# Optimization experiments

Measured on AMD Instinct MI355X. Metric: run time of the kernel, lower is better.

The kernel has to match this reference:

```python
import jax, jax.numpy as jnp
import numpy as np

N = 20000
E = 320000
CIN = 16
COUT = 16
D = 4
RADIUS = 0.5


def setup_inputs() -> dict:
    key = jax.random.key(0)
    k1, k2, k3, k4 = jax.random.split(key, 4)
    positions = jax.random.uniform(k1, (N, 3), dtype=jnp.float32)
    features = jax.random.normal(k2, (N, CIN), dtype=jnp.float32)
    filters = jax.random.normal(k3, (D, D, D, CIN, COUT), dtype=jnp.float32)
    edge_index = jax.random.randint(k4, (2, E), 0, N, dtype=jnp.int32)
    return {"positions": positions, "features": features,
            "filters": filters, "edge_index": edge_index}


def _trilinear(filters, gc):
    # Replicates torch grid_sample(align_corners=True) semantics used by the
    # module: grid coord (x,y,z) indexes spatial dims (W,H,D), i.e. gc[:,0]
    # samples filter axis 2, gc[:,1] axis 1, gc[:,2] axis 0.
    Dres = filters.shape[0]
    a, b, c = gc[:, 2], gc[:, 1], gc[:, 0]  # axes 0, 1, 2 of filters
    a0f, b0f, c0f = jnp.floor(a), jnp.floor(b), jnp.floor(c)
    a0 = jnp.clip(a0f.astype(jnp.int32), 0, Dres - 1)
    b0 = jnp.clip(b0f.astype(jnp.int32), 0, Dres - 1)
    c0 = jnp.clip(c0f.astype(jnp.int32), 0, Dres - 1)
    a1 = jnp.minimum(a0 + 1, Dres - 1)
    b1 = jnp.minimum(b0 + 1, Dres - 1)
    c1 = jnp.minimum(c0 + 1, Dres - 1)
    ad = (a - a0f)[:, None, None]  # (E,1,1)
    bd = (b - b0f)[:, None, None]
    cd = (c - c0f)[:, None, None]

    g = lambda i, j, k: filters[i, j, k]  # (E, CIN, COUT) gather
    f00 = g(a0, b0, c0) * (1 - cd) + g(a0, b0, c1) * cd
    f01 = g(a0, b1, c0) * (1 - cd) + g(a0, b1, c1) * cd
    f10 = g(a1, b0, c0) * (1 - cd) + g(a1, b0, c1) * cd
    f11 = g(a1, b1, c0) * (1 - cd) + g(a1, b1, c1) * cd
    f0 = f00 * (1 - bd) + f01 * bd
    f1 = f10 * (1 - bd) + f11 * bd
    return f0 * (1 - ad) + f1 * ad  # (E, CIN, COUT)


def reference(positions, features, filters, edge_index):
    row, col = edge_index[0], edge_index[1]
    r = positions[col] - positions[row]                  # (E,3)
    dist2 = jnp.sum(r * r, axis=-1)                      # (E,)
    valid = (dist2 < RADIUS ** 2).astype(positions.dtype)
    window = (1.0 - dist2 / RADIUS ** 2) ** 3 * valid
    norm = jnp.sqrt(dist2)[:, None]
    mapped = r / (norm + 1e-8) * jnp.tanh(norm)          # ball -> cube, (E,3)
    gc = (mapped + 1.0) * ((filters.shape[0] - 1) / 2.0) # (E,3) in [0, D-1]
    filt = _trilinear(filters, gc)                       # (E, CIN, COUT)
    conv_edge = jnp.einsum('eio,ei->eo', filt, features[col])
    conv_edge = conv_edge * window[:, None]
    n_nodes = positions.shape[0]
    sums = jax.ops.segment_sum(conv_edge, row, num_segments=n_nodes)
    cnt = jax.ops.segment_sum(jnp.ones((conv_edge.shape[0],), positions.dtype),
                              row, num_segments=n_nodes)
    return sums / jnp.maximum(cnt, 1.0)[:, None]         # scatter-mean
```

## Files before the change

kernel.cpp:

```cpp
#include <hip/hip_runtime.h>
#include <hip/hip_fp16.h>
#include <math.h>

#define NN 20000
#define EE 320000
#define CIN 16
#define COUT 16
#define R2C 0.25f

#define WS_NEED 81920

typedef _Float16 h2 __attribute__((ext_vector_type(2)));

#if defined(__has_builtin)
# if __has_builtin(__builtin_amdgcn_fdot2)
#  define HAS_FDOT2 1
# endif
#endif
#ifndef HAS_FDOT2
# define HAS_FDOT2 0
#endif

__device__ __forceinline__ h2 as_h2(unsigned int x) {
    union { unsigned int u; h2 h; } v; v.u = x; return v.h;
}
__device__ __forceinline__ h2 pk(float a, float b) {
    h2 r; r.x = (_Float16)a; r.y = (_Float16)b; return r;
}
__device__ __forceinline__ unsigned int pku(float a, float b) {
    __half2 h = __float22half2_rn(make_float2(a, b));
    return *(unsigned int*)&h;
}

__global__ __launch_bounds__(256) void k_zero(float* __restrict__ out, int* __restrict__ cnt) {
    int i = blockIdx.x * 256 + threadIdx.x;
    if (i < NN * COUT) out[i] = 0.0f;
    if (i < NN) cnt[i] = 0;
}

__global__ __launch_bounds__(256) void k_edge(const float* __restrict__ pos,
                                              const int* __restrict__ ei,
                                              const float* __restrict__ feat,
                                              const float* __restrict__ filt,
                                              float* __restrict__ out,
                                              int* __restrict__ cnts) {
    __shared__ uint4 sf[2048];
    {
        #pragma unroll
        for (int r = 0; r < 8; ++r) {
            int g = r * 256 + threadIdx.x;
            const float* src = filt + (g >> 4) * 128 + (g & 15);
            float s0 = src[0],  s1 = src[16],  s2 = src[32],  s3 = src[48];
            float s4 = src[64], s5 = src[80],  s6 = src[96],  s7 = src[112];
            uint4 v;
            v.x = pku(s0, s1); v.y = pku(s2, s3);
            v.z = pku(s4, s5); v.w = pku(s6, s7);
            sf[g] = v;
        }
    }
    __syncthreads();

    int lane = threadIdx.x & 63;
    int gid  = lane >> 4;
    int o    = lane & 15;
    int wv   = threadIdx.x >> 6;

    #pragma unroll
    for (int ch = 0; ch < 2; ++ch) {
        int e = blockIdx.x * 512 + ch * 256 + wv * 64 + lane;

        int row = ei[e];
        int col = ei[EE + e];
        atomicAdd(&cnts[row], 1);

        float rx = pos[col*3+0] - pos[row*3+0];
        float ry = pos[col*3+1] - pos[row*3+1];
        float rz = pos[col*3+2] - pos[row*3+2];
        float d2 = rx*rx + ry*ry + rz*rz;
        bool valid = d2 < R2C;

        float win = 0.f, ad = 0.f, bd = 0.f, cd = 0.f;
        int colidx = 0;
        if (valid) {
            float u = 1.0f - d2 * 4.0f;
            win = u * u * u;
            float s = 1.0f + d2*(-0.33333333f + d2*(0.13333333f + d2*(-0.05396825f + d2*0.02186949f)));
            float gx = (rx * s + 1.0f) * 1.5f;
            float gy = (ry * s + 1.0f) * 1.5f;
            float gz = (rz * s + 1.0f) * 1.5f;
            float af = floorf(gz), bf = floorf(gy), cf = floorf(gx);
            int ia0 = min(max((int)af, 0), 2);
            int jb0 = min(max((int)bf, 0), 2);
            int kc0 = min(max((int)cf, 0), 2);
            ad = gz - af; bd = gy - bf; cd = gx - cf;
            colidx = col | (ia0 << 20) | (jb0 << 24) | (kc0 << 28);
        }

        unsigned long long bal = __ballot(valid);
        int nv = __popcll(bal);
        unsigned long long m0 = bal;
        unsigned long long m1 = m0 & (m0 - 1);
        unsigned long long m2 = m1 & (m1 - 1);
        unsigned long long m3 = m2 & (m2 - 1);

        for (int k = 0; k < nv; k += 4) {
            unsigned long long mg = (gid == 0) ? m0 : (gid == 1) ? m1 : (gid == 2) ? m2 : m3;
            bool active = (k + gid) < nv;
            int src = active ? (int)__builtin_ctzll(mg) : 0;

            float win_s = __shfl(win, src, 64);
            float ad_s  = __shfl(ad,  src, 64);
            float bd_s  = __shfl(bd,  src, 64);
            float cd_s  = __shfl(cd,  src, 64);
            int   ci_s  = __shfl(colidx, src, 64);
            int   row_s = __shfl(row,    src, 64);

            m0 = m3 & (m3 - 1);
            m1 = m0 & (m0 - 1);
            m2 = m1 & (m1 - 1);
            m3 = m2 & (m2 - 1);

            if (active) {
                int col_s = ci_s & 0xFFFFF;
                int ia0 = (ci_s >> 20) & 3, jb0 = (ci_s >> 24) & 3, kc0 = (ci_s >> 28) & 3;

                const float4* fb = (const float4*)(feat + (size_t)col_s * 16);
                float4 fa = fb[0], fc = fb[1], fd = fb[2], fe = fb[3];

                float va0 = (1.f - ad_s) * win_s, va1 = ad_s * win_s;
                float vb0 = 1.f - bd_s, vb1 = bd_s;
                float vc0 = 1.f - cd_s, vc1 = cd_s;
                float p00 = va0*vb0, p01 = va0*vb1, p10 = va1*vb0, p11 = va1*vb1;
                float w8[8] = { p00*vc0, p00*vc1, p01*vc0, p01*vc1,
                                p10*vc0, p10*vc1, p11*vc0, p11*vc1 };

                int bi = ((ia0 * 16 + jb0 * 4 + kc0) << 5) + o;
                const int cofs[8] = {0, 32, 128, 160, 512, 544, 640, 672};

                float acc = 0.f;
#if HAS_FDOT2
                h2 ft0 = pk(fa.x, fa.y), ft1 = pk(fa.z, fa.w);
                h2 ft2 = pk(fc.x, fc.y), ft3 = pk(fc.z, fc.w);
                h2 ft4 = pk(fd.x, fd.y), ft5 = pk(fd.z, fd.w);
                h2 ft6 = pk(fe.x, fe.y), ft7 = pk(fe.z, fe.w);
                #pragma unroll
                for (int c = 0; c < 8; ++c) {
                    uint4 g0 = sf[bi + cofs[c]];
                    uint4 g1 = sf[bi + cofs[c] + 16];
                    float d = 0.f;
                    d = __builtin_amdgcn_fdot2(as_h2(g0.x), ft0, d, false);
                    d = __builtin_amdgcn_fdot2(as_h2(g0.y), ft1, d, false);
                    d = __builtin_amdgcn_fdot2(as_h2(g0.z), ft2, d, false);
                    d = __builtin_amdgcn_fdot2(as_h2(g0.w), ft3, d, false);
                    d = __builtin_amdgcn_fdot2(as_h2(g1.x), ft4, d, false);
                    d = __builtin_amdgcn_fdot2(as_h2(g1.y), ft5, d, false);
                    d = __builtin_amdgcn_fdot2(as_h2(g1.z), ft6, d, false);
                    d = __builtin_amdgcn_fdot2(as_h2(g1.w), ft7, d, false);
                    acc = fmaf(w8[c], d, acc);
                }
#else
                float ftf[16] = { fa.x, fa.y, fa.z, fa.w, fc.x, fc.y, fc.z, fc.w,
                                  fd.x, fd.y, fd.z, fd.w, fe.x, fe.y, fe.z, fe.w };
                #pragma unroll
                for (int c = 0; c < 8; ++c) {
                    uint4 g0 = sf[bi + cofs[c]];
                    uint4 g1 = sf[bi + cofs[c] + 16];
                    float d = 0.f;
                    h2 t;
                    t = as_h2(g0.x); d = fmaf((float)t.x, ftf[0],  d); d = fmaf((float)t.y, ftf[1],  d);
                    t = as_h2(g0.y); d = fmaf((float)t.x, ftf[2],  d); d = fmaf((float)t.y, ftf[3],  d);
                    t = as_h2(g0.z); d = fmaf((float)t.x, ftf[4],  d); d = fmaf((float)t.y, ftf[5],  d);
                    t = as_h2(g0.w); d = fmaf((float)t.x, ftf[6],  d); d = fmaf((float)t.y, ftf[7],  d);
                    t = as_h2(g1.x); d = fmaf((float)t.x, ftf[8],  d); d = fmaf((float)t.y, ftf[9],  d);
                    t = as_h2(g1.y); d = fmaf((float)t.x, ftf[10], d); d = fmaf((float)t.y, ftf[11], d);
                    t = as_h2(g1.z); d = fmaf((float)t.x, ftf[12], d); d = fmaf((float)t.y, ftf[13], d);
                    t = as_h2(g1.w); d = fmaf((float)t.x, ftf[14], d); d = fmaf((float)t.y, ftf[15], d);
                    acc = fmaf(w8[c], d, acc);
                }
#endif
                atomicAdd(out + (size_t)row_s * 16 + o, acc);
            }
        }
    }
}

__global__ __launch_bounds__(256) void k_div(float* __restrict__ out, const int* __restrict__ cnt) {
    int i = blockIdx.x * 256 + threadIdx.x;
    if (i >= NN * COUT) return;
    int c = cnt[i >> 4];
    float denom = (c > 1) ? (float)c : 1.0f;
    out[i] = out[i] / denom;
}

__device__ __forceinline__ bool edge_geom(const float* __restrict__ pos, int row, int col,
                                          float& win,
                                          int ia[2], int jb[2], int kc[2],
                                          float wa[2], float wb[2], float wc[2]) {
    float rx = pos[col*3+0] - pos[row*3+0];
    float ry = pos[col*3+1] - pos[row*3+1];
    float rz = pos[col*3+2] - pos[row*3+2];
    float d2 = rx*rx + ry*ry + rz*rz;
    if (!(d2 < R2C)) return false;
    float u = 1.0f - d2 / R2C;
    win = u * u * u;
    float nr = sqrtf(d2);
    float s  = tanhf(nr) / (nr + 1e-8f);
    float gx = (rx * s + 1.0f) * 1.5f;
    float gy = (ry * s + 1.0f) * 1.5f;
    float gz = (rz * s + 1.0f) * 1.5f;
    float af = floorf(gz), bf = floorf(gy), cf = floorf(gx);
    int ia0 = min(max((int)af, 0), 3);
    int ib0 = min(max((int)bf, 0), 3);
    int ic0 = min(max((int)cf, 0), 3);
    ia[0] = ia0; ia[1] = min(ia0 + 1, 3);
    jb[0] = ib0; jb[1] = min(ib0 + 1, 3);
    kc[0] = ic0; kc[1] = min(ic0 + 1, 3);
    float ad = gz - af, bd = gy - bf, cd = gx - cf;
    wa[0] = 1.0f - ad; wa[1] = ad;
    wb[0] = 1.0f - bd; wb[1] = bd;
    wc[0] = 1.0f - cd; wc[1] = cd;
    return true;
}

__global__ __launch_bounds__(256) void k_edge_direct(const float* __restrict__ pos,
                                                     const float* __restrict__ feat,
                                                     const float* __restrict__ filt,
                                                     const int* __restrict__ ei,
                                                     float* __restrict__ out,
                                                     int* __restrict__ cnt) {
    int e = blockIdx.x * 256 + threadIdx.x;
    if (e >= EE) return;
    int row = ei[e];
    int col = ei[EE + e];
    atomicAdd(&cnt[row], 1);

    float win;
    int ia[2], jb[2], kc[2];
    float wa[2], wb[2], wc[2];
    if (!edge_geom(pos, row, col, win, ia, jb, kc, wa, wb, wc)) return;

    float fv[16];
    const float4* fp = (const float4*)(feat + (size_t)col * 16);
    float4 f0 = fp[0], f1 = fp[1], f2 = fp[2], f3 = fp[3];
    fv[0]=f0.x; fv[1]=f0.y; fv[2]=f0.z; fv[3]=f0.w;
    fv[4]=f1.x; fv[5]=f1.y; fv[6]=f1.z; fv[7]=f1.w;
    fv[8]=f2.x; fv[9]=f2.y; fv[10]=f2.z; fv[11]=f2.w;
    fv[12]=f3.x; fv[13]=f3.y; fv[14]=f3.z; fv[15]=f3.w;

    float4 a0 = make_float4(0.f,0.f,0.f,0.f);
    float4 a1 = a0, a2 = a0, a3 = a0;
    for (int da = 0; da < 2; ++da)
    for (int db = 0; db < 2; ++db)
    for (int dc = 0; dc < 2; ++dc) {
        float w = wa[da] * wb[db] * wc[dc] * win;
        const float* fb = filt + (size_t)(ia[da]*16 + jb[db]*4 + kc[dc]) * 256;
        #pragma unroll
        for (int ci = 0; ci < 16; ++ci) {
            float c = w * fv[ci];
            const float4* r4 = (const float4*)(fb + ci * 16);
            float4 w0 = r4[0], w1 = r4[1], w2 = r4[2], w3 = r4[3];
            a0.x = fmaf(c, w0.x, a0.x); a0.y = fmaf(c, w0.y, a0.y);
            a0.z = fmaf(c, w0.z, a0.z); a0.w = fmaf(c, w0.w, a0.w);
            a1.x = fmaf(c, w1.x, a1.x); a1.y = fmaf(c, w1.y, a1.y);
            a1.z = fmaf(c, w1.z, a1.z); a1.w = fmaf(c, w1.w, a1.w);
            a2.x = fmaf(c, w2.x, a2.x); a2.y = fmaf(c, w2.y, a2.y);
            a2.z = fmaf(c, w2.z, a2.z); a2.w = fmaf(c, w2.w, a2.w);
            a3.x = fmaf(c, w3.x, a3.x); a3.y = fmaf(c, w3.y, a3.y);
            a3.z = fmaf(c, w3.z, a3.z); a3.w = fmaf(c, w3.w, a3.w);
        }
    }
    float* op = out + (size_t)row * 16;
    atomicAdd(op+0,  a0.x); atomicAdd(op+1,  a0.y); atomicAdd(op+2,  a0.z); atomicAdd(op+3,  a0.w);
    atomicAdd(op+4,  a1.x); atomicAdd(op+5,  a1.y); atomicAdd(op+6,  a1.z); atomicAdd(op+7,  a1.w);
    atomicAdd(op+8,  a2.x); atomicAdd(op+9,  a2.y); atomicAdd(op+10, a2.z); atomicAdd(op+11, a2.w);
    atomicAdd(op+12, a3.x); atomicAdd(op+13, a3.y); atomicAdd(op+14, a3.z); atomicAdd(op+15, a3.w);
}

extern "C" void kernel_launch(void* const* d_in, const int* in_sizes, int n_in,
                              void* d_out, int out_size, void* d_ws, size_t ws_size,
                              hipStream_t stream) {
    const float* pos  = (const float*)d_in[0];
    const float* feat = (const float*)d_in[1];
    const float* filt = (const float*)d_in[2];
    const int*   ei   = (const int*)d_in[3];
    float* out = (float*)d_out;

    int* cnts = (int*)d_ws;

    k_zero<<<(NN * COUT + 255) / 256, 256, 0, stream>>>(out, cnts);
    if (ws_size >= WS_NEED) {
        k_edge<<<625, 256, 0, stream>>>(pos, ei, feat, filt, out, cnts);
    } else {
        k_edge_direct<<<(EE + 255) / 256, 256, 0, stream>>>(pos, feat, filt, ei, out, cnts);
    }
    k_div<<<(NN * COUT + 255) / 256, 256, 0, stream>>>(out, cnts);
}
```

Baseline: 92.02 us.

## Prefetch edge indices before filter staging and software-pipeline lane shuffles

Edge index loads and count atomics for both 256-edge chunks are now issued before and alongside the shared-memory filter staging, so their global latency overlaps the LDS fill. Geometry for both chunks is computed up front, which lets the position gathers of the second chunk overlap with the first. Inside the compaction loop, the shuffles for the next round are issued before the current round's work, which hides cross-lane latency. The cost is higher register pressure from holding two edge states and the double-buffered shuffled values.

```diff
diff --git a/kernel.cpp b/kernel.cpp
--- a/kernel.cpp
+++ b/kernel.cpp
@@ -38,6 +38,142 @@
     if (i < NN) cnt[i] = 0;
 }
 
+struct EdgeSt {
+    float win, ad, bd, cd;
+    int colidx, row;
+    unsigned long long bal;
+};
+
+__device__ __forceinline__ void geom(const float* __restrict__ pos, int row, int col,
+                                     EdgeSt& st) {
+    float rx = pos[col*3+0] - pos[row*3+0];
+    float ry = pos[col*3+1] - pos[row*3+1];
+    float rz = pos[col*3+2] - pos[row*3+2];
+    float d2 = rx*rx + ry*ry + rz*rz;
+    bool valid = d2 < R2C;
+    st.win = 0.f; st.ad = 0.f; st.bd = 0.f; st.cd = 0.f; st.colidx = 0; st.row = row;
+    if (valid) {
+        float u = 1.0f - d2 * 4.0f;
+        st.win = u * u * u;
+        float s = 1.0f + d2*(-0.33333333f + d2*(0.13333333f + d2*(-0.05396825f + d2*0.02186949f)));
+        float gx = (rx * s + 1.0f) * 1.5f;
+        float gy = (ry * s + 1.0f) * 1.5f;
+        float gz = (rz * s + 1.0f) * 1.5f;
+        float af = floorf(gz), bf = floorf(gy), cf = floorf(gx);
+        int ia0 = min(max((int)af, 0), 2);
+        int jb0 = min(max((int)bf, 0), 2);
+        int kc0 = min(max((int)cf, 0), 2);
+        st.ad = gz - af; st.bd = gy - bf; st.cd = gx - cf;
+        st.colidx = col | (ia0 << 20) | (jb0 << 24) | (kc0 << 28);
+    }
+    st.bal = __ballot(valid);
+}
+
+__device__ __forceinline__ void conv_rounds(const EdgeSt& st,
+                                            const uint4* __restrict__ sf,
+                                            const float* __restrict__ feat,
+                                            float* __restrict__ out,
+                                            int gid, int o) {
+    unsigned long long bal = st.bal;
+    int nv = __popcll(bal);
+    if (nv == 0) return;
+
+    unsigned long long m0 = bal;
+    unsigned long long m1 = m0 & (m0 - 1);
+    unsigned long long m2 = m1 & (m1 - 1);
+    unsigned long long m3 = m2 & (m2 - 1);
+
+    unsigned long long mg = (gid == 0) ? m0 : (gid == 1) ? m1 : (gid == 2) ? m2 : m3;
+    int src = mg ? (int)__builtin_ctzll(mg) : 0;
+    float win_s = __shfl(st.win, src, 64);
+    float ad_s  = __shfl(st.ad,  src, 64);
+    float bd_s  = __shfl(st.bd,  src, 64);
+    float cd_s  = __shfl(st.cd,  src, 64);
+    int   ci_s  = __shfl(st.colidx, src, 64);
+    int   row_s = __shfl(st.row,    src, 64);
+
+    for (int k = 0; k < nv; k += 4) {
+        m0 = m3 & (m3 - 1);
+        m1 = m0 & (m0 - 1);
+        m2 = m1 & (m1 - 1);
+        m3 = m2 & (m2 - 1);
+        unsigned long long mg2 = (gid == 0) ? m0 : (gid == 1) ? m1 : (gid == 2) ? m2 : m3;
+        int src2 = mg2 ? (int)__builtin_ctzll(mg2) : 0;
+
+        bool active = (k + gid) < nv;
+        float winc = win_s, adc = ad_s, bdc = bd_s, cdc = cd_s;
+        int   cic = ci_s, rowc = row_s;
+
+        win_s = __shfl(st.win, src2, 64);
+        ad_s  = __shfl(st.ad,  src2, 64);
+        bd_s  = __shfl(st.bd,  src2, 64);
+        cd_s  = __shfl(st.cd,  src2, 64);
+        ci_s  = __shfl(st.colidx, src2, 64);
+        row_s = __shfl(st.row,    src2, 64);
+
+        if (active) {
+            int col_s = cic & 0xFFFFF;
+            int ia0 = (cic >> 20) & 3, jb0 = (cic >> 24) & 3, kc0 = (cic >> 28) & 3;
+
+            const float4* fb = (const float4*)(feat + (size_t)col_s * 16);
+            float4 fa = fb[0], fc = fb[1], fd = fb[2], fe = fb[3];
+
+            float va0 = (1.f - adc) * winc, va1 = adc * winc;
+            float vb0 = 1.f - bdc, vb1 = bdc;
+            float vc0 = 1.f - cdc, vc1 = cdc;
+            float p00 = va0*vb0, p01 = va0*vb1, p10 = va1*vb0, p11 = va1*vb1;
+            float w8[8] = { p00*vc0, p00*vc1, p01*vc0, p01*vc1,
+                            p10*vc0, p10*vc1, p11*vc0, p11*vc1 };
+
+            int bi = ((ia0 * 16 + jb0 * 4 + kc0) << 5) + o;
+            const int cofs[8] = {0, 32, 128, 160, 512, 544, 640, 672};
+
+            float acc = 0.f;
+#if HAS_FDOT2
+            h2 ft0 = pk(fa.x, fa.y), ft1 = pk(fa.z, fa.w);
+            h2 ft2 = pk(fc.x, fc.y), ft3 = pk(fc.z, fc.w);
+            h2 ft4 = pk(fd.x, fd.y), ft5 = pk(fd.z, fd.w);
+            h2 ft6 = pk(fe.x, fe.y), ft7 = pk(fe.z, fe.w);
+            #pragma unroll
+            for (int c = 0; c < 8; ++c) {
+                uint4 g0 = sf[bi + cofs[c]];
+                uint4 g1 = sf[bi + cofs[c] + 16];
+                float d = 0.f;
+                d = __builtin_amdgcn_fdot2(as_h2(g0.x), ft0, d, false);
+                d = __builtin_amdgcn_fdot2(as_h2(g0.y), ft1, d, false);
+                d = __builtin_amdgcn_fdot2(as_h2(g0.z), ft2, d, false);
+                d = __builtin_amdgcn_fdot2(as_h2(g0.w), ft3, d, false);
+                d = __builtin_amdgcn_fdot2(as_h2(g1.x), ft4, d, false);
+                d = __builtin_amdgcn_fdot2(as_h2(g1.y), ft5, d, false);
+                d = __builtin_amdgcn_fdot2(as_h2(g1.z), ft6, d, false);
+                d = __builtin_amdgcn_fdot2(as_h2(g1.w), ft7, d, false);
+                acc = fmaf(w8[c], d, acc);
+            }
+#else
+            float ftf[16] = { fa.x, fa.y, fa.z, fa.w, fc.x, fc.y, fc.z, fc.w,
+                              fd.x, fd.y, fd.z, fd.w, fe.x, fe.y, fe.z, fe.w };
+            #pragma unroll
+            for (int c = 0; c < 8; ++c) {
+                uint4 g0 = sf[bi + cofs[c]];
+                uint4 g1 = sf[bi + cofs[c] + 16];
+                float d = 0.f;
+                h2 t;
+                t = as_h2(g0.x); d = fmaf((float)t.x, ftf[0],  d); d = fmaf((float)t.y, ftf[1],  d);
+                t = as_h2(g0.y); d = fmaf((float)t.x, ftf[2],  d); d = fmaf((float)t.y, ftf[3],  d);
+                t = as_h2(g0.z); d = fmaf((float)t.x, ftf[4],  d); d = fmaf((float)t.y, ftf[5],  d);
+                t = as_h2(g0.w); d = fmaf((float)t.x, ftf[6],  d); d = fmaf((float)t.y, ftf[7],  d);
+                t = as_h2(g1.x); d = fmaf((float)t.x, ftf[8],  d); d = fmaf((float)t.y, ftf[9],  d);
+                t = as_h2(g1.y); d = fmaf((float)t.x, ftf[10], d); d = fmaf((float)t.y, ftf[11], d);
+                t = as_h2(g1.z); d = fmaf((float)t.x, ftf[12], d); d = fmaf((float)t.y, ftf[13], d);
+                t = as_h2(g1.w); d = fmaf((float)t.x, ftf[14], d); d = fmaf((float)t.y, ftf[15], d);
+                acc = fmaf(w8[c], d, acc);
+            }
+#endif
+            atomicAdd(out + (size_t)rowc * 16 + o, acc);
+        }
+    }
+}
+
 __global__ __launch_bounds__(256) void k_edge(const float* __restrict__ pos,
                                               const int* __restrict__ ei,
                                               const float* __restrict__ feat,
@@ -45,6 +181,20 @@
                                               float* __restrict__ out,
                                               int* __restrict__ cnts) {
     __shared__ uint4 sf[2048];
+
+    int lane = threadIdx.x & 63;
+    int gid  = lane >> 4;
+    int o    = lane & 15;
+    int wv   = threadIdx.x >> 6;
+
+    int e0 = blockIdx.x * 512 + wv * 64 + lane;
+    int e1 = e0 + 256;
+
+    int row0 = ei[e0];
+    int col0 = ei[EE + e0];
+    int row1 = ei[e1];
+    int col1 = ei[EE + e1];
+
     {
         #pragma unroll
         for (int r = 0; r < 8; ++r) {
@@ -58,130 +208,18 @@
             sf[g] = v;
         }
     }
+
+    atomicAdd(&cnts[row0], 1);
+    atomicAdd(&cnts[row1], 1);
+
     __syncthreads();
 
-    int lane = threadIdx.x & 63;
-    int gid  = lane >> 4;
-    int o    = lane & 15;
-    int wv   = threadIdx.x >> 6;
-
-    #pragma unroll
-    for (int ch = 0; ch < 2; ++ch) {
-        int e = blockIdx.x * 512 + ch * 256 + wv * 64 + lane;
-
-        int row = ei[e];
-        int col = ei[EE + e];
-        atomicAdd(&cnts[row], 1);
-
-        float rx = pos[col*3+0] - pos[row*3+0];
-        float ry = pos[col*3+1] - pos[row*3+1];
-        float rz = pos[col*3+2] - pos[row*3+2];
-        float d2 = rx*rx + ry*ry + rz*rz;
-        bool valid = d2 < R2C;
-
-        float win = 0.f, ad = 0.f, bd = 0.f, cd = 0.f;
-        int colidx = 0;
-        if (valid) {
-            float u = 1.0f - d2 * 4.0f;
-            win = u * u * u;
-            float s = 1.0f + d2*(-0.33333333f + d2*(0.13333333f + d2*(-0.05396825f + d2*0.02186949f)));
-            float gx = (rx * s + 1.0f) * 1.5f;
-            float gy = (ry * s + 1.0f) * 1.5f;
-            float gz = (rz * s + 1.0f) * 1.5f;
-            float af = floorf(gz), bf = floorf(gy), cf = floorf(gx);
-            int ia0 = min(max((int)af, 0), 2);
-            int jb0 = min(max((int)bf, 0), 2);
-            int kc0 = min(max((int)cf, 0), 2);
-            ad = gz - af; bd = gy - bf; cd = gx - cf;
-            colidx = col | (ia0 << 20) | (jb0 << 24) | (kc0 << 28);
-        }
-
-        unsigned long long bal = __ballot(valid);
-        int nv = __popcll(bal);
-        unsigned long long m0 = bal;
-        unsigned long long m1 = m0 & (m0 - 1);
-        unsigned long long m2 = m1 & (m1 - 1);
-        unsigned long long m3 = m2 & (m2 - 1);
-
-        for (int k = 0; k < nv; k += 4) {
-            unsigned long long mg = (gid == 0) ? m0 : (gid == 1) ? m1 : (gid == 2) ? m2 : m3;
-            bool active = (k + gid) < nv;
-            int src = active ? (int)__builtin_ctzll(mg) : 0;
-
-            float win_s = __shfl(win, src, 64);
-            float ad_s  = __shfl(ad,  src, 64);
-            float bd_s  = __shfl(bd,  src, 64);
-            float cd_s  = __shfl(cd,  src, 64);
-            int   ci_s  = __shfl(colidx, src, 64);
-            int   row_s = __shfl(row,    src, 64);
-
-            m0 = m3 & (m3 - 1);
-            m1 = m0 & (m0 - 1);
-            m2 = m1 & (m1 - 1);
-            m3 = m2 & (m2 - 1);
-
-            if (active) {
-                int col_s = ci_s & 0xFFFFF;
-                int ia0 = (ci_s >> 20) & 3, jb0 = (ci_s >> 24) & 3, kc0 = (ci_s >> 28) & 3;
-
-                const float4* fb = (const float4*)(feat + (size_t)col_s * 16);
-                float4 fa = fb[0], fc = fb[1], fd = fb[2], fe = fb[3];
-
-                float va0 = (1.f - ad_s) * win_s, va1 = ad_s * win_s;
-                float vb0 = 1.f - bd_s, vb1 = bd_s;
-                float vc0 = 1.f - cd_s, vc1 = cd_s;
-                float p00 = va0*vb0, p01 = va0*vb1, p10 = va1*vb0, p11 = va1*vb1;
-                float w8[8] = { p00*vc0, p00*vc1, p01*vc0, p01*vc1,
-                                p10*vc0, p10*vc1, p11*vc0, p11*vc1 };
-
-                int bi = ((ia0 * 16 + jb0 * 4 + kc0) << 5) + o;
-                const int cofs[8] = {0, 32, 128, 160, 512, 544, 640, 672};
-
-                float acc = 0.f;
-#if HAS_FDOT2
-                h2 ft0 = pk(fa.x, fa.y), ft1 = pk(fa.z, fa.w);
-                h2 ft2 = pk(fc.x, fc.y), ft3 = pk(fc.z, fc.w);
-                h2 ft4 = pk(fd.x, fd.y), ft5 = pk(fd.z, fd.w);
-                h2 ft6 = pk(fe.x, fe.y), ft7 = pk(fe.z, fe.w);
-                #pragma unroll
-                for (int c = 0; c < 8; ++c) {
-                    uint4 g0 = sf[bi + cofs[c]];
-                    uint4 g1 = sf[bi + cofs[c] + 16];
-                    float d = 0.f;
-                    d = __builtin_amdgcn_fdot2(as_h2(g0.x), ft0, d, false);
-                    d = __builtin_amdgcn_fdot2(as_h2(g0.y), ft1, d, false);
-                    d = __builtin_amdgcn_fdot2(as_h2(g0.z), ft2, d, false);
-                    d = __builtin_amdgcn_fdot2(as_h2(g0.w), ft3, d, false);
-                    d = __builtin_amdgcn_fdot2(as_h2(g1.x), ft4, d, false);
-                    d = __builtin_amdgcn_fdot2(as_h2(g1.y), ft5, d, false);
-                    d = __builtin_amdgcn_fdot2(as_h2(g1.z), ft6, d, false);
-                    d = __builtin_amdgcn_fdot2(as_h2(g1.w), ft7, d, false);
-                    acc = fmaf(w8[c], d, acc);
-                }
-#else
-                float ftf[16] = { fa.x, fa.y, fa.z, fa.w, fc.x, fc.y, fc.z, fc.w,
-                                  fd.x, fd.y, fd.z, fd.w, fe.x, fe.y, fe.z, fe.w };
-                #pragma unroll
-                for (int c = 0; c < 8; ++c) {
-                    uint4 g0 = sf[bi + cofs[c]];
-                    uint4 g1 = sf[bi + cofs[c] + 16];
-                    float d = 0.f;
-                    h2 t;
-                    t = as_h2(g0.x); d = fmaf((float)t.x, ftf[0],  d); d = fmaf((float)t.y, ftf[1],  d);
-                    t = as_h2(g0.y); d = fmaf((float)t.x, ftf[2],  d); d = fmaf((float)t.y, ftf[3],  d);
-                    t = as_h2(g0.z); d = fmaf((float)t.x, ftf[4],  d); d = fmaf((float)t.y, ftf[5],  d);
-                    t = as_h2(g0.w); d = fmaf((float)t.x, ftf[6],  d); d = fmaf((float)t.y, ftf[7],  d);
-                    t = as_h2(g1.x); d = fmaf((float)t.x, ftf[8],  d); d = fmaf((float)t.y, ftf[9],  d);
-                    t = as_h2(g1.y); d = fmaf((float)t.x, ftf[10], d); d = fmaf((float)t.y, ftf[11], d);
-                    t = as_h2(g1.z); d = fmaf((float)t.x, ftf[12], d); d = fmaf((float)t.y, ftf[13], d);
-                    t = as_h2(g1.w); d = fmaf((float)t.x, ftf[14], d); d = fmaf((float)t.y, ftf[15], d);
-                    acc = fmaf(w8[c], d, acc);
-                }
-#endif
-                atomicAdd(out + (size_t)row_s * 16 + o, acc);
-            }
-        }
-    }
+    EdgeSt st0, st1;
+    geom(pos, row0, col0, st0);
+    geom(pos, row1, col1, st1);
+
+    conv_rounds(st0, sf, feat, out, gid, o);
+    conv_rounds(st1, sf, feat, out, gid, o);
 }
 
 __global__ __launch_bounds__(256) void k_div(float* __restrict__ out, const int* __restrict__ cnt) {
```

Result: slower. 96.20 us (+4.5%).

## Fuse zero, edge, and divide kernels into one cooperative kernel with grid syncs

Applied to the files above, without the earlier changes.

Merges the zero-init, edge scatter, and mean-divide kernels into a single cooperative launch of 625 blocks, separated by grid-wide barriers. Each thread zeroes and later divides a float2 slice of the output, which covers all 320000 floats exactly. The aim is to remove two kernel launches and the gaps between them. The cost is two grid.sync barriers and a cap of 3 blocks per CU from the launch bounds, and the cooperative launch may fail and fall back to the old three-kernel path.

```diff
diff --git a/kernel.cpp b/kernel.cpp
--- a/kernel.cpp
+++ b/kernel.cpp
@@ -1,5 +1,6 @@
 #include <hip/hip_runtime.h>
 #include <hip/hip_fp16.h>
+#include <hip/hip_cooperative_groups.h>
 #include <math.h>
 
 #define NN 20000
@@ -32,19 +33,14 @@
     return *(unsigned int*)&h;
 }
 
-__global__ __launch_bounds__(256) void k_zero(float* __restrict__ out, int* __restrict__ cnt) {
-    int i = blockIdx.x * 256 + threadIdx.x;
-    if (i < NN * COUT) out[i] = 0.0f;
-    if (i < NN) cnt[i] = 0;
-}
-
-__global__ __launch_bounds__(256) void k_edge(const float* __restrict__ pos,
-                                              const int* __restrict__ ei,
-                                              const float* __restrict__ feat,
-                                              const float* __restrict__ filt,
-                                              float* __restrict__ out,
-                                              int* __restrict__ cnts) {
-    __shared__ uint4 sf[2048];
+__device__ __forceinline__ void edge_body(const float* __restrict__ pos,
+                                          const int* __restrict__ ei,
+                                          const float* __restrict__ feat,
+                                          const float* __restrict__ filt,
+                                          float* __restrict__ out,
+                                          int* __restrict__ cnts,
+                                          uint4* __restrict__ sf,
+                                          int bid) {
     {
         #pragma unroll
         for (int r = 0; r < 8; ++r) {
@@ -67,7 +63,7 @@
 
     #pragma unroll
     for (int ch = 0; ch < 2; ++ch) {
-        int e = blockIdx.x * 512 + ch * 256 + wv * 64 + lane;
+        int e = bid * 512 + ch * 256 + wv * 64 + lane;
 
         int row = ei[e];
         int col = ei[EE + e];
@@ -184,6 +180,50 @@
     }
 }
 
+__global__ __launch_bounds__(256, 3) void k_fused(const float* __restrict__ pos,
+                                                  const int* __restrict__ ei,
+                                                  const float* __restrict__ feat,
+                                                  const float* __restrict__ filt,
+                                                  float* __restrict__ out,
+                                                  int* __restrict__ cnts) {
+    __shared__ uint4 sf[2048];
+    cooperative_groups::grid_group grid = cooperative_groups::this_grid();
+
+    int t = blockIdx.x * 256 + threadIdx.x;
+
+    ((float2*)out)[t] = make_float2(0.f, 0.f);
+    if (t < NN) cnts[t] = 0;
+
+    grid.sync();
+
+    edge_body(pos, ei, feat, filt, out, cnts, sf, blockIdx.x);
+
+    grid.sync();
+
+    {
+        int c = cnts[t >> 3];
+        float inv = (c > 1) ? 1.0f / (float)c : 1.0f;
+        float2 v = ((float2*)out)[t];
+        ((float2*)out)[t] = make_float2(v.x * inv, v.y * inv);
+    }
+}
+
+__global__ __launch_bounds__(256) void k_zero(float* __restrict__ out, int* __restrict__ cnt) {
+    int i = blockIdx.x * 256 + threadIdx.x;
+    if (i < NN * COUT) out[i] = 0.0f;
+    if (i < NN) cnt[i] = 0;
+}
+
+__global__ __launch_bounds__(256) void k_edge(const float* __restrict__ pos,
+                                              const int* __restrict__ ei,
+                                              const float* __restrict__ feat,
+                                              const float* __restrict__ filt,
+                                              float* __restrict__ out,
+                                              int* __restrict__ cnts) {
+    __shared__ uint4 sf[2048];
+    edge_body(pos, ei, feat, filt, out, cnts, sf, blockIdx.x);
+}
+
 __global__ __launch_bounds__(256) void k_div(float* __restrict__ out, const int* __restrict__ cnt) {
     int i = blockIdx.x * 256 + threadIdx.x;
     if (i >= NN * COUT) return;
@@ -287,11 +327,18 @@
 
     int* cnts = (int*)d_ws;
 
-    k_zero<<<(NN * COUT + 255) / 256, 256, 0, stream>>>(out, cnts);
     if (ws_size >= WS_NEED) {
+        void* args[] = { (void*)&pos, (void*)&ei, (void*)&feat, (void*)&filt,
+                         (void*)&out, (void*)&cnts };
+        hipError_t err = hipLaunchCooperativeKernel((void*)k_fused, dim3(625), dim3(256),
+                                                    args, 0, stream);
+        if (err == hipSuccess) return;
+        k_zero<<<(NN * COUT + 255) / 256, 256, 0, stream>>>(out, cnts);
         k_edge<<<625, 256, 0, stream>>>(pos, ei, feat, filt, out, cnts);
+        k_div<<<(NN * COUT + 255) / 256, 256, 0, stream>>>(out, cnts);
     } else {
+        k_zero<<<(NN * COUT + 255) / 256, 256, 0, stream>>>(out, cnts);
         k_edge_direct<<<(EE + 255) / 256, 256, 0, stream>>>(pos, feat, filt, ei, out, cnts);
-    }
-    k_div<<<(NN * COUT + 255) / 256, 256, 0, stream>>>(out, cnts);
-}
+        k_div<<<(NN * COUT + 255) / 256, 256, 0, stream>>>(out, cnts);
+    }
+}
```

Result: slower. 218.8 us (+137.8%).
